# Kernel optimization log

Hardware: AMD Instinct MI355X
Metric: run time of the kernel (lower is better)

## Reference

```python
import jax, jax.numpy as jnp
import numpy as np

K = 10  # top-k from __init__ kwarg k


def _gru_cell(x, h, w_ih, w_hh, b_ih, b_hh):
    # torch nn.GRUCell gate order: r, z, n
    gi = x @ w_ih.T + b_ih
    gh = h @ w_hh.T + b_hh
    ir, iz, in_ = jnp.split(gi, 3, axis=-1)
    hr, hz, hn = jnp.split(gh, 3, axis=-1)
    r = jax.nn.sigmoid(ir + hr)
    z = jax.nn.sigmoid(iz + hz)
    n = jnp.tanh(in_ + r * hn)
    return (1.0 - z) * n + z * h


def setup_inputs() -> dict:
    key = jax.random.key(0)
    ks = jax.random.split(key, 10)
    B, V, H, L = 16, 50000, 512, 2
    E = H  # embedding_dim must equal rnn_size (embedding feeds GRU input)
    interesting = (jax.random.uniform(ks[0], (B, V)) < 0.01).astype(jnp.float32)
    masking = jnp.ones((B, V), jnp.float32)
    emb = jax.random.normal(ks[1], (V, E), jnp.float32) * 0.02
    s = 1.0 / np.sqrt(H)
    gw_ih = jax.random.normal(ks[2], (L, 3 * H, H), jnp.float32) * s
    gw_hh = jax.random.normal(ks[3], (L, 3 * H, H), jnp.float32) * s
    gb_ih = jax.random.normal(ks[4], (L, 3 * H), jnp.float32) * s
    gb_hh = jax.random.normal(ks[5], (L, 3 * H), jnp.float32) * s
    fc_w = jax.random.normal(ks[6], (V, H), jnp.float32) * s
    fc_b = jax.random.normal(ks[7], (V,), jnp.float32) * s
    value_w = jax.random.normal(ks[8], (1, H), jnp.float32) * s
    value_b = jax.random.normal(ks[9], (1,), jnp.float32) * s
    return {
        'user_interesting': interesting, 'user_masking': masking,
        'embedding': emb,
        'gru_w_ih': gw_ih, 'gru_w_hh': gw_hh, 'gru_b_ih': gb_ih, 'gru_b_hh': gb_hh,
        'fc_w': fc_w, 'fc_b': fc_b, 'value_w': value_w, 'value_b': value_b,
        'sequence_length': 32,
    }


def reference(user_interesting, user_masking, embedding, gru_w_ih, gru_w_hh,
              gru_b_ih, gru_b_hh, fc_w, fc_b, value_w, value_b, sequence_length):
    B, V = user_interesting.shape
    L, H = gru_w_ih.shape[0], value_w.shape[1]
    T = int(sequence_length)
    dt = user_interesting.dtype
    s_token, s_hit = 0, 1.0
    # NOTE (faithful to source): SimpleGRUCell.forward returns the OLD hidden
    # as new_state, so the recurrent state stays at its zero init every step.
    h0 = jnp.zeros((B, H), dt)
    # start inputs: embedding(start_token) * start_hit, broadcast over batch
    # (in torch the [1,E] input broadcasts against [B,H] hidden inside GRUCell;
    #  since hidden is zero this equals broadcasting the input to B).
    start_inputs = jnp.broadcast_to(embedding[s_token] * s_hit, (B, embedding.shape[1]))
    bidx = jnp.arange(B)[:, None]

    def step(carry, _):
        inputs, history = carry
        x = inputs
        for l in range(L):  # stacked GRU cells, hidden always zero (see note)
            x = _gru_cell(x, h0, gru_w_ih[l], gru_w_hh[l], gru_b_ih[l], gru_b_hh[l])
        policy = jax.nn.softmax(x @ fc_w.T + fc_b, axis=-1)        # [B,V]
        value = x @ value_w.T + value_b                             # [B,1]
        masked = policy * history
        _, topk_idx = jax.lax.top_k(masked, K)                      # [B,K]
        oh_topk = jnp.zeros_like(policy).at[bidx, topk_idx].set(1.0)
        cii = user_interesting * oh_topk
        hff = (jnp.sum(cii, axis=-1) > 0).astype(dt)[:, None]       # hit flag [B,1]
        score = hff * cii * policy + (1.0 - hff) * masked
        sel = jnp.argmax(score, axis=-1)                            # [B]
        oh_sel = jnp.zeros_like(policy).at[bidx, sel[:, None]].set(1.0)
        emb = embedding[sel]                                        # [B,E]
        next_inputs = hff * emb + (hff - 1.0) * emb                 # = (2*hff-1)*emb
        next_history = history - hff * oh_sel
        return (next_inputs, next_history), (policy, sel, value, hff)

    (_, final_history), (pol, sel, val, hit) = jax.lax.scan(
        step, (start_inputs, user_masking), None, length=T)
    # time-major -> batch-major
    logits = jnp.swapaxes(pol, 0, 1)        # [B,T,V]
    sample_ids = jnp.swapaxes(sel, 0, 1)    # [B,T]
    values = jnp.swapaxes(val, 0, 1)        # [B,T,1]
    hits = jnp.swapaxes(hit, 0, 1)          # [B,T,1]
    return logits, sample_ids, values, final_history, hits
```

## Files before the change

### kernel.cpp

```cpp
#include <hip/hip_runtime.h>


#define TT 32
#define BDIM 16
#define VD 50000
#define HD 512
#define NB3 782

#define WS_HIST 0
#define WS_X0   800000
#define WS_X1   808192
#define WS_X2T  816384
#define WS_SWS  824576
#define WS_TV   837088
#define WS_INVS 962208
#define WS_TI   962224
#define WS_FCWT 1088000

#define O_IDS 25600000
#define O_VAL 25600512
#define O_FH  25601024
#define O_HIT 26401024

__global__ __launch_bounds__(256) void k_init(const float4* __restrict__ mask4,
                                              const float4* __restrict__ emb4,
                                              float4* __restrict__ hist4,
                                              float4* __restrict__ x04)
{
    for (int idx = blockIdx.x * 256 + threadIdx.x; idx < 202048; idx += 256 * 256) {
        if (idx < 200000) hist4[idx] = mask4[idx];
        else { int c = idx - 200000; x04[c] = emb4[c & 127]; }
    }
}

__global__ __launch_bounds__(256) void k_transpose(const float* __restrict__ src,
                                                   float* __restrict__ dst)
{
    __shared__ float tile[64][65];
    const int bt = blockIdx.x, tv = bt >> 3, th = bt & 7;
    const int v0 = tv * 64, h0 = th * 64;
    const int tx = threadIdx.x & 63, ty4 = threadIdx.x >> 6;
    for (int p = 0; p < 16; p++) {
        int vr = p * 4 + ty4, v = v0 + vr;
        tile[vr][tx] = (v < VD) ? src[(size_t)v * HD + h0 + tx] : 0.f;
    }
    __syncthreads();
    for (int p = 0; p < 16; p++) {
        int hr = p * 4 + ty4, v = v0 + tx;
        if (v < VD) dst[(size_t)(h0 + hr) * VD + v] = tile[tx][hr];
    }
}

__global__ __launch_bounds__(256) void k_gru(const float* __restrict__ xin,
                                             float* __restrict__ xout,
                                             const float* __restrict__ W,
                                             const float* __restrict__ bi,
                                             const float* __restrict__ bh,
                                             int outT,
                                             float* __restrict__ dout,
                                             const float* __restrict__ invS,
                                             int tprev)
{
    if (blockIdx.x >= 128) {
        if (tprev < 0) return;
        for (int idx = (blockIdx.x - 128) * 256 + threadIdx.x; idx < 200000; idx += 256 * 256) {
            int b = idx / 12500, v4 = idx % 12500;
            float4* row = (float4*)(dout + ((size_t)b * TT + tprev) * VD);
            float4 e = row[v4]; float s = invS[b];
            e.x *= s; e.y *= s; e.z *= s; e.w *= s;
            row[v4] = e;
        }
        return;
    }
    const int tid = threadIdx.x;
    const int kq = tid & 3, b = (tid >> 2) & 15, jl = tid >> 6;
    const int j = blockIdx.x * 4 + jl;
    const float4* xr = (const float4*)(xin + (size_t)b * HD + kq * 128);
    const float4* wr = (const float4*)(W + (size_t)j * HD + kq * 128);
    const float4* wz = (const float4*)(W + (size_t)(j + 512) * HD + kq * 128);
    const float4* wn = (const float4*)(W + (size_t)(j + 1024) * HD + kq * 128);
    float4 aR = {0, 0, 0, 0}, aZ = {0, 0, 0, 0}, aN = {0, 0, 0, 0};
#pragma unroll 4
    for (int k = 0; k < 32; k++) {
        float4 x = xr[k];
        float4 r = wr[k];
        aR.x = fmaf(r.x, x.x, aR.x); aR.y = fmaf(r.y, x.y, aR.y);
        aR.z = fmaf(r.z, x.z, aR.z); aR.w = fmaf(r.w, x.w, aR.w);
        float4 z = wz[k];
        aZ.x = fmaf(z.x, x.x, aZ.x); aZ.y = fmaf(z.y, x.y, aZ.y);
        aZ.z = fmaf(z.z, x.z, aZ.z); aZ.w = fmaf(z.w, x.w, aZ.w);
        float4 n = wn[k];
        aN.x = fmaf(n.x, x.x, aN.x); aN.y = fmaf(n.y, x.y, aN.y);
        aN.z = fmaf(n.z, x.z, aN.z); aN.w = fmaf(n.w, x.w, aN.w);
    }
    float sR = (aR.x + aR.y) + (aR.z + aR.w);
    float sZ = (aZ.x + aZ.y) + (aZ.z + aZ.w);
    float sN = (aN.x + aN.y) + (aN.z + aN.w);
    sR += __shfl_xor(sR, 1, 64); sR += __shfl_xor(sR, 2, 64);
    sZ += __shfl_xor(sZ, 1, 64); sZ += __shfl_xor(sZ, 2, 64);
    sN += __shfl_xor(sN, 1, 64); sN += __shfl_xor(sN, 2, 64);
    if (kq == 0) {
        float gr = sR + bi[j] + bh[j];
        float gz = sZ + bi[512 + j] + bh[512 + j];
        float rr = 1.f / (1.f + expf(-gr));
        float zz = 1.f / (1.f + expf(-gz));
        float nn = tanhf(sN + bi[1024 + j] + rr * bh[1024 + j]);
        float o = (1.f - zz) * nn;
        if (outT) xout[(size_t)j * 16 + b] = o;
        else      xout[(size_t)b * HD + j] = o;
    }
}

template<int TRANS>
__global__ __launch_bounds__(256, 4) void k3_fc(const float* __restrict__ W,
                                                const float* __restrict__ fcb,
                                                const float* __restrict__ x2T,
                                                const float* __restrict__ hist,
                                                float* __restrict__ dout,
                                                float* __restrict__ s_ws,
                                                float* __restrict__ tv_ws,
                                                int* __restrict__ ti_ws,
                                                int t)
{
    __shared__ float red[4][64][17];
    __shared__ float elds[64][17];
    const int tid = threadIdx.x;
    const int wave = tid >> 6, lane = tid & 63;
    const int khu = __builtin_amdgcn_readfirstlane(wave);
    const int vb0 = blockIdx.x * 64;
    const int v = vb0 + lane;
    float acc[16];
#pragma unroll
    for (int i = 0; i < 16; i++) acc[i] = 0.f;
    const float* xp = x2T + khu * 128 * 16;
    if (v < VD) {
        if (TRANS) {
            const float* wp = W + (size_t)(khu * 128) * VD + v;
#pragma unroll 4
            for (int k = 0; k < 128; k++) {
                float w = wp[(size_t)k * VD];
                const float* xr = xp + k * 16;
#pragma unroll
                for (int bb = 0; bb < 16; bb++) acc[bb] = fmaf(w, xr[bb], acc[bb]);
            }
        } else {
            const float4* wp = (const float4*)(W + (size_t)v * HD + khu * 128);
#pragma unroll 2
            for (int k4 = 0; k4 < 32; k4++) {
                float4 w = wp[k4];
                const float* xr = xp + k4 * 64;
#pragma unroll
                for (int bb = 0; bb < 16; bb++) acc[bb] = fmaf(w.x, xr[bb], acc[bb]);
#pragma unroll
                for (int bb = 0; bb < 16; bb++) acc[bb] = fmaf(w.y, xr[16 + bb], acc[bb]);
#pragma unroll
                for (int bb = 0; bb < 16; bb++) acc[bb] = fmaf(w.z, xr[32 + bb], acc[bb]);
#pragma unroll
                for (int bb = 0; bb < 16; bb++) acc[bb] = fmaf(w.w, xr[48 + bb], acc[bb]);
            }
        }
    }
#pragma unroll
    for (int i = 0; i < 16; i++) red[khu][lane][i] = acc[i];
    __syncthreads();

    const int v_l = tid & 63;
    const int vglob = vb0 + v_l;
    const int bq = (tid >> 6) * 4;
    float fb = (vglob < VD) ? fcb[vglob] : 0.f;
#pragma unroll
    for (int q = 0; q < 4; q++) {
        int bb = bq + q;
        float lg = (red[0][v_l][bb] + red[1][v_l][bb]) + (red[2][v_l][bb] + red[3][v_l][bb]);
        float e = 0.f;
        if (vglob < VD) {
            e = expf(lg + fb);
            dout[((size_t)bb * TT + t) * VD + vglob] = e;
        }
        elds[v_l][bb] = e;
    }
    __syncthreads();

    for (int q = 0; q < 4; q++) {
        int bb = wave * 4 + q;
        float e0 = elds[lane][bb];
        float s = e0;
#pragma unroll
        for (int m = 1; m < 64; m <<= 1) s += __shfl_xor(s, m, 64);
        int i0 = vb0 + lane;
        float h0 = (i0 < VD) ? hist[(size_t)bb * VD + i0] : 0.f;
        float k0 = e0 * h0;
        for (int r = 0; r < 10; r++) {
            float cvv = k0; int cii = i0;
#pragma unroll
            for (int m = 1; m < 64; m <<= 1) {
                float ov = __shfl_xor(cvv, m, 64);
                int   oi = __shfl_xor(cii, m, 64);
                if (ov > cvv || (ov == cvv && oi < cii)) { cvv = ov; cii = oi; }
            }
            if (lane == 0) {
                size_t o = ((size_t)blockIdx.x * 16 + bb) * 10 + r;
                tv_ws[o] = cvv; ti_ws[o] = cii;
            }
            if (cii == i0) k0 = -1.f;
        }
        if (lane == 0) s_ws[blockIdx.x * 16 + bb] = s;
    }
}

__global__ __launch_bounds__(256) void k5_merge(const float* __restrict__ s_ws,
                                                const float* __restrict__ tv_ws,
                                                const int* __restrict__ ti_ws,
                                                const float* __restrict__ ui,
                                                const float* __restrict__ emb,
                                                const float* __restrict__ x2T,
                                                const float* __restrict__ vw,
                                                const float* __restrict__ vbias,
                                                float* __restrict__ hist,
                                                float* __restrict__ x0,
                                                float* __restrict__ dout,
                                                float* __restrict__ invS,
                                                int t)
{
    const int b = blockIdx.x, tid = threadIdx.x;
    __shared__ float cv[7824];
    __shared__ unsigned short ci16[7824];
    __shared__ float rv[256]; __shared__ int ri[256]; __shared__ int rs[256];
    __shared__ float t10v[10]; __shared__ int t10i[10];
    __shared__ float ifl[10], ev[10];
    __shared__ int s_sel; __shared__ float s_hff;

    for (int c = tid; c < 7820; c += 256) {
        int j = c / 10, r = c % 10;
        cv[c] = tv_ws[((size_t)j * 16 + b) * 10 + r];
        ci16[c] = (unsigned short)ti_ws[((size_t)j * 16 + b) * 10 + r];
    }
    if (tid < 4) { cv[7820 + tid] = -1e30f; ci16[7820 + tid] = 65535; }
    __syncthreads();

    for (int r = 0; r < 10; r++) {
        float bv = -1e30f; int bi = 0x7fffffff, bs = 0;
        for (int c = tid; c < 7820; c += 256) {
            float vv = cv[c]; int ii = (int)ci16[c];
            if (vv > bv || (vv == bv && ii < bi)) { bv = vv; bi = ii; bs = c; }
        }
        rv[tid] = bv; ri[tid] = bi; rs[tid] = bs;
        __syncthreads();
        for (int s = 128; s > 0; s >>= 1) {
            if (tid < s) {
                float ov = rv[tid + s]; int oi = ri[tid + s];
                if (ov > rv[tid] || (ov == rv[tid] && oi < ri[tid])) {
                    rv[tid] = ov; ri[tid] = oi; rs[tid] = rs[tid + s];
                }
            }
            __syncthreads();
        }
        if (tid == 0) { t10v[r] = rv[0]; t10i[r] = ri[0]; cv[rs[0]] = -1e30f; }
        __syncthreads();
    }

    float sp = 0.f;
    for (int c = tid; c < NB3; c += 256) sp += s_ws[c * 16 + b];
    rv[tid] = sp; __syncthreads();
    for (int s = 128; s > 0; s >>= 1) { if (tid < s) rv[tid] += rv[tid + s]; __syncthreads(); }
    float S = rv[0];
    __syncthreads();

    float vp = x2T[(size_t)tid * 16 + b] * vw[tid] + x2T[(size_t)(tid + 256) * 16 + b] * vw[tid + 256];
    rv[tid] = vp; __syncthreads();
    for (int s = 128; s > 0; s >>= 1) { if (tid < s) rv[tid] += rv[tid + s]; __syncthreads(); }

    if (tid < 10) {
        int ii = t10i[tid];
        ifl[tid] = ui[(size_t)b * VD + ii];
        ev[tid] = dout[((size_t)b * TT + t) * VD + ii];
    }
    __syncthreads();

    if (tid == 0) {
        int hff = 0; float bv = -1e30f; int bsel = -1;
        for (int r = 0; r < 10; r++) {
            if (ifl[r] != 0.f) {
                if (!hff || ev[r] > bv) { bv = ev[r]; bsel = t10i[r]; }
                hff = 1;
            }
        }
        int sel = hff ? bsel : t10i[0];
        s_sel = sel; s_hff = (float)hff;
        dout[O_IDS + b * TT + t] = (float)sel;
        dout[O_HIT + b * TT + t] = (float)hff;
        dout[O_VAL + b * TT + t] = rv[0] + vbias[0];
        invS[b] = 1.f / S;
        if (hff) hist[(size_t)b * VD + sel] -= 1.f;
    }
    __syncthreads();
    float f = 2.f * s_hff - 1.f;
    x0[(size_t)b * HD + tid]       = f * emb[(size_t)s_sel * HD + tid];
    x0[(size_t)b * HD + tid + 256] = f * emb[(size_t)s_sel * HD + tid + 256];
}

__global__ __launch_bounds__(256) void k_final(float* __restrict__ dout,
                                               const float4* __restrict__ hist4,
                                               const float* __restrict__ invS)
{
    for (int idx = blockIdx.x * 256 + threadIdx.x; idx < 400000; idx += 256 * 256) {
        if (idx < 200000) {
            int b = idx / 12500, v4 = idx % 12500;
            float4* row = (float4*)(dout + ((size_t)b * TT + 31) * VD);
            float4 e = row[v4]; float s = invS[b];
            e.x *= s; e.y *= s; e.z *= s; e.w *= s;
            row[v4] = e;
        } else {
            int c = idx - 200000;
            ((float4*)(dout + O_FH))[c] = hist4[c];
        }
    }
}

extern "C" void kernel_launch(void* const* d_in, const int* in_sizes, int n_in,
                              void* d_out, int out_size, void* d_ws, size_t ws_size,
                              hipStream_t stream)
{
    const float* ui   = (const float*)d_in[0];
    const float* mask = (const float*)d_in[1];
    const float* emb  = (const float*)d_in[2];
    const float* wih  = (const float*)d_in[3];
    const float* gbih = (const float*)d_in[5];
    const float* gbhh = (const float*)d_in[6];
    const float* fcw  = (const float*)d_in[7];
    const float* fcb  = (const float*)d_in[8];
    const float* vw   = (const float*)d_in[9];
    const float* vb   = (const float*)d_in[10];
    float* out = (float*)d_out;

    float* wsf  = (float*)d_ws;
    float* hist = wsf + WS_HIST;
    float* x0   = wsf + WS_X0;
    float* x1   = wsf + WS_X1;
    float* x2T  = wsf + WS_X2T;
    float* sws  = wsf + WS_SWS;
    float* tvws = wsf + WS_TV;
    float* invS = wsf + WS_INVS;
    int*   tiws = (int*)(wsf + WS_TI);
    float* fcwT = wsf + WS_FCWT;
    const bool use_t = ws_size >= (size_t)(WS_FCWT + (size_t)HD * VD) * 4;

    k_init<<<256, 256, 0, stream>>>((const float4*)mask, (const float4*)emb,
                                    (float4*)hist, (float4*)x0);
    if (use_t) k_transpose<<<6256, 256, 0, stream>>>(fcw, fcwT);

    for (int t = 0; t < TT; t++) {
        k_gru<<<384, 256, 0, stream>>>(x0, x1, wih, gbih, gbhh, 0, out, invS, t - 1);
        k_gru<<<128, 256, 0, stream>>>(x1, x2T, wih + 786432, gbih + 1536, gbhh + 1536,
                                       1, out, invS, -1);
        if (use_t) k3_fc<1><<<NB3, 256, 0, stream>>>(fcwT, fcb, x2T, hist, out, sws, tvws, tiws, t);
        else       k3_fc<0><<<NB3, 256, 0, stream>>>(fcw,  fcb, x2T, hist, out, sws, tvws, tiws, t);
        k5_merge<<<16, 256, 0, stream>>>(sws, tvws, tiws, ui, emb, x2T, vw, vb,
                                         hist, x0, out, invS, t);
    }
    k_final<<<256, 256, 0, stream>>>(out, (const float4*)hist, invS);
}
```

Baseline: 4.421 ms.

## Fuse layer-0 GRU into merge kernel and replace tree reductions with wave shuffles

Folds the first GRU layer of the next step into the top-k merge kernel. The 16 per-batch merge blocks become 64 blocks, each handling a quarter of the GRU output rows, so one kernel launch per step is removed and the selected embedding stays in shared memory. The previous-step logits rescale moves into the same kernel, and the step-0 layer-0 GRU moves into the init kernel. The shared-memory tree argmax reduction is replaced with wavefront shuffle reductions, which cuts barrier count. The cost is that each batch's top-10 selection is now computed four times redundantly.

```diff
diff --git a/kernel.cpp b/kernel.cpp
--- a/kernel.cpp
+++ b/kernel.cpp
@@ -2,13 +2,11 @@
 
 
 #define TT 32
-#define BDIM 16
 #define VD 50000
 #define HD 512
 #define NB3 782
 
 #define WS_HIST 0
-#define WS_X0   800000
 #define WS_X1   808192
 #define WS_X2T  816384
 #define WS_SWS  824576
@@ -23,13 +21,53 @@
 #define O_HIT 26401024
 
 __global__ __launch_bounds__(256) void k_init(const float4* __restrict__ mask4,
-                                              const float4* __restrict__ emb4,
                                               float4* __restrict__ hist4,
-                                              float4* __restrict__ x04)
-{
-    for (int idx = blockIdx.x * 256 + threadIdx.x; idx < 202048; idx += 256 * 256) {
-        if (idx < 200000) hist4[idx] = mask4[idx];
-        else { int c = idx - 200000; x04[c] = emb4[c & 127]; }
+                                              const float* __restrict__ emb,
+                                              const float* __restrict__ W,
+                                              const float* __restrict__ bi,
+                                              const float* __restrict__ bh,
+                                              float* __restrict__ x1)
+{
+    if (blockIdx.x < 256) {
+        for (int idx = blockIdx.x * 256 + threadIdx.x; idx < 200000; idx += 256 * 256)
+            hist4[idx] = mask4[idx];
+        return;
+    }
+    const int bid2 = blockIdx.x - 256;
+    const int tid = threadIdx.x;
+    const int kq = tid & 3, b = (tid >> 2) & 15, jl = tid >> 6;
+    const int j = bid2 * 4 + jl;
+    const float4* xr = (const float4*)(emb + kq * 128);
+    const float4* wr = (const float4*)(W + (size_t)j * HD + kq * 128);
+    const float4* wz = (const float4*)(W + (size_t)(j + 512) * HD + kq * 128);
+    const float4* wn = (const float4*)(W + (size_t)(j + 1024) * HD + kq * 128);
+    float4 aR = {0, 0, 0, 0}, aZ = {0, 0, 0, 0}, aN = {0, 0, 0, 0};
+#pragma unroll 4
+    for (int k = 0; k < 32; k++) {
+        float4 x = xr[k];
+        float4 r = wr[k];
+        aR.x = fmaf(r.x, x.x, aR.x); aR.y = fmaf(r.y, x.y, aR.y);
+        aR.z = fmaf(r.z, x.z, aR.z); aR.w = fmaf(r.w, x.w, aR.w);
+        float4 z = wz[k];
+        aZ.x = fmaf(z.x, x.x, aZ.x); aZ.y = fmaf(z.y, x.y, aZ.y);
+        aZ.z = fmaf(z.z, x.z, aZ.z); aZ.w = fmaf(z.w, x.w, aZ.w);
+        float4 n = wn[k];
+        aN.x = fmaf(n.x, x.x, aN.x); aN.y = fmaf(n.y, x.y, aN.y);
+        aN.z = fmaf(n.z, x.z, aN.z); aN.w = fmaf(n.w, x.w, aN.w);
+    }
+    float sR = (aR.x + aR.y) + (aR.z + aR.w);
+    float sZ = (aZ.x + aZ.y) + (aZ.z + aZ.w);
+    float sN = (aN.x + aN.y) + (aN.z + aN.w);
+    sR += __shfl_xor(sR, 1, 64); sR += __shfl_xor(sR, 2, 64);
+    sZ += __shfl_xor(sZ, 1, 64); sZ += __shfl_xor(sZ, 2, 64);
+    sN += __shfl_xor(sN, 1, 64); sN += __shfl_xor(sN, 2, 64);
+    if (kq == 0) {
+        float gr = sR + bi[j] + bh[j];
+        float gz = sZ + bi[512 + j] + bh[512 + j];
+        float rr = 1.f / (1.f + expf(-gr));
+        float zz = 1.f / (1.f + expf(-gz));
+        float nn = tanhf(sN + bi[1024 + j] + rr * bh[1024 + j]);
+        x1[(size_t)b * HD + j] = (1.f - zz) * nn;
     }
 }
 
@@ -51,27 +89,12 @@
     }
 }
 
-__global__ __launch_bounds__(256) void k_gru(const float* __restrict__ xin,
-                                             float* __restrict__ xout,
-                                             const float* __restrict__ W,
-                                             const float* __restrict__ bi,
-                                             const float* __restrict__ bh,
-                                             int outT,
-                                             float* __restrict__ dout,
-                                             const float* __restrict__ invS,
-                                             int tprev)
-{
-    if (blockIdx.x >= 128) {
-        if (tprev < 0) return;
-        for (int idx = (blockIdx.x - 128) * 256 + threadIdx.x; idx < 200000; idx += 256 * 256) {
-            int b = idx / 12500, v4 = idx % 12500;
-            float4* row = (float4*)(dout + ((size_t)b * TT + tprev) * VD);
-            float4 e = row[v4]; float s = invS[b];
-            e.x *= s; e.y *= s; e.z *= s; e.w *= s;
-            row[v4] = e;
-        }
-        return;
-    }
+__global__ __launch_bounds__(256) void k_gru1(const float* __restrict__ xin,
+                                              float* __restrict__ xout,
+                                              const float* __restrict__ W,
+                                              const float* __restrict__ bi,
+                                              const float* __restrict__ bh)
+{
     const int tid = threadIdx.x;
     const int kq = tid & 3, b = (tid >> 2) & 15, jl = tid >> 6;
     const int j = blockIdx.x * 4 + jl;
@@ -105,9 +128,7 @@
         float rr = 1.f / (1.f + expf(-gr));
         float zz = 1.f / (1.f + expf(-gz));
         float nn = tanhf(sN + bi[1024 + j] + rr * bh[1024 + j]);
-        float o = (1.f - zz) * nn;
-        if (outT) xout[(size_t)j * 16 + b] = o;
-        else      xout[(size_t)b * HD + j] = o;
+        xout[(size_t)j * 16 + b] = (1.f - zz) * nn;
     }
 }
 
@@ -208,72 +229,96 @@
     }
 }
 
-__global__ __launch_bounds__(256) void k5_merge(const float* __restrict__ s_ws,
-                                                const float* __restrict__ tv_ws,
-                                                const int* __restrict__ ti_ws,
-                                                const float* __restrict__ ui,
-                                                const float* __restrict__ emb,
-                                                const float* __restrict__ x2T,
-                                                const float* __restrict__ vw,
-                                                const float* __restrict__ vbias,
-                                                float* __restrict__ hist,
-                                                float* __restrict__ x0,
-                                                float* __restrict__ dout,
-                                                float* __restrict__ invS,
-                                                int t)
-{
-    const int b = blockIdx.x, tid = threadIdx.x;
+__global__ __launch_bounds__(256) void k_mergeall(const float* __restrict__ s_ws,
+                                                  const float* __restrict__ tv_ws,
+                                                  const int* __restrict__ ti_ws,
+                                                  const float* __restrict__ ui,
+                                                  const float* __restrict__ emb,
+                                                  const float* __restrict__ x2T,
+                                                  const float* __restrict__ vw,
+                                                  const float* __restrict__ vbias,
+                                                  float* __restrict__ hist,
+                                                  float* __restrict__ x1out,
+                                                  const float* __restrict__ W0,
+                                                  const float* __restrict__ bi0,
+                                                  const float* __restrict__ bh0,
+                                                  float* __restrict__ dout,
+                                                  float* __restrict__ invS,
+                                                  int t)
+{
+    const int tid = threadIdx.x;
+    if (blockIdx.x >= 64) {
+        if (t == 0) return;
+        for (int idx = (blockIdx.x - 64) * 256 + tid; idx < 200000; idx += 256 * 256) {
+            int b = idx / 12500, v4 = idx % 12500;
+            float4* row = (float4*)(dout + ((size_t)b * TT + (t - 1)) * VD);
+            float4 e = row[v4]; float s = invS[b];
+            e.x *= s; e.y *= s; e.z *= s; e.w *= s;
+            row[v4] = e;
+        }
+        return;
+    }
+    const int b = blockIdx.x >> 2, jq = blockIdx.x & 3;
     __shared__ float cv[7824];
     __shared__ unsigned short ci16[7824];
-    __shared__ float rv[256]; __shared__ int ri[256]; __shared__ int rs[256];
+    __shared__ float rv[256];
+    __shared__ float wbv[4]; __shared__ int wbi[4]; __shared__ int wbs[4];
     __shared__ float t10v[10]; __shared__ int t10i[10];
     __shared__ float ifl[10], ev[10];
     __shared__ int s_sel; __shared__ float s_hff;
+    __shared__ __align__(16) float x0b[512];
 
     for (int c = tid; c < 7820; c += 256) {
         int j = c / 10, r = c % 10;
         cv[c] = tv_ws[((size_t)j * 16 + b) * 10 + r];
         ci16[c] = (unsigned short)ti_ws[((size_t)j * 16 + b) * 10 + r];
     }
-    if (tid < 4) { cv[7820 + tid] = -1e30f; ci16[7820 + tid] = 65535; }
-    __syncthreads();
-
+    __syncthreads();
+
+    const int lane = tid & 63, wv = tid >> 6;
     for (int r = 0; r < 10; r++) {
         float bv = -1e30f; int bi = 0x7fffffff, bs = 0;
         for (int c = tid; c < 7820; c += 256) {
             float vv = cv[c]; int ii = (int)ci16[c];
             if (vv > bv || (vv == bv && ii < bi)) { bv = vv; bi = ii; bs = c; }
         }
-        rv[tid] = bv; ri[tid] = bi; rs[tid] = bs;
+#pragma unroll
+        for (int m = 1; m < 64; m <<= 1) {
+            float ov = __shfl_xor(bv, m, 64);
+            int   oi = __shfl_xor(bi, m, 64);
+            int   os = __shfl_xor(bs, m, 64);
+            if (ov > bv || (ov == bv && oi < bi)) { bv = ov; bi = oi; bs = os; }
+        }
+        if (lane == 0) { wbv[wv] = bv; wbi[wv] = bi; wbs[wv] = bs; }
         __syncthreads();
-        for (int s = 128; s > 0; s >>= 1) {
-            if (tid < s) {
-                float ov = rv[tid + s]; int oi = ri[tid + s];
-                if (ov > rv[tid] || (ov == rv[tid] && oi < ri[tid])) {
-                    rv[tid] = ov; ri[tid] = oi; rs[tid] = rs[tid + s];
-                }
-            }
-            __syncthreads();
-        }
-        if (tid == 0) { t10v[r] = rv[0]; t10i[r] = ri[0]; cv[rs[0]] = -1e30f; }
+        if (tid == 0) {
+            float fv = wbv[0]; int fi = wbi[0], fs = wbs[0];
+#pragma unroll
+            for (int w = 1; w < 4; w++)
+                if (wbv[w] > fv || (wbv[w] == fv && wbi[w] < fi)) { fv = wbv[w]; fi = wbi[w]; fs = wbs[w]; }
+            t10v[r] = fv; t10i[r] = fi; cv[fs] = -1e30f;
+        }
         __syncthreads();
     }
 
-    float sp = 0.f;
-    for (int c = tid; c < NB3; c += 256) sp += s_ws[c * 16 + b];
-    rv[tid] = sp; __syncthreads();
-    for (int s = 128; s > 0; s >>= 1) { if (tid < s) rv[tid] += rv[tid + s]; __syncthreads(); }
-    float S = rv[0];
-    __syncthreads();
-
-    float vp = x2T[(size_t)tid * 16 + b] * vw[tid] + x2T[(size_t)(tid + 256) * 16 + b] * vw[tid + 256];
-    rv[tid] = vp; __syncthreads();
-    for (int s = 128; s > 0; s >>= 1) { if (tid < s) rv[tid] += rv[tid + s]; __syncthreads(); }
+    float S_reg = 0.f;
+    if (jq == 0) {
+        float sp = 0.f;
+        for (int c = tid; c < NB3; c += 256) sp += s_ws[c * 16 + b];
+        rv[tid] = sp; __syncthreads();
+        for (int s = 128; s > 0; s >>= 1) { if (tid < s) rv[tid] += rv[tid + s]; __syncthreads(); }
+        S_reg = rv[0];
+        __syncthreads();
+        float vp = x2T[(size_t)tid * 16 + b] * vw[tid]
+                 + x2T[(size_t)(tid + 256) * 16 + b] * vw[tid + 256];
+        rv[tid] = vp; __syncthreads();
+        for (int s = 128; s > 0; s >>= 1) { if (tid < s) rv[tid] += rv[tid + s]; __syncthreads(); }
+    }
 
     if (tid < 10) {
         int ii = t10i[tid];
         ifl[tid] = ui[(size_t)b * VD + ii];
-        ev[tid] = dout[((size_t)b * TT + t) * VD + ii];
+        ev[tid]  = dout[((size_t)b * TT + t) * VD + ii];
     }
     __syncthreads();
 
@@ -287,16 +332,60 @@
         }
         int sel = hff ? bsel : t10i[0];
         s_sel = sel; s_hff = (float)hff;
-        dout[O_IDS + b * TT + t] = (float)sel;
-        dout[O_HIT + b * TT + t] = (float)hff;
-        dout[O_VAL + b * TT + t] = rv[0] + vbias[0];
-        invS[b] = 1.f / S;
-        if (hff) hist[(size_t)b * VD + sel] -= 1.f;
-    }
-    __syncthreads();
-    float f = 2.f * s_hff - 1.f;
-    x0[(size_t)b * HD + tid]       = f * emb[(size_t)s_sel * HD + tid];
-    x0[(size_t)b * HD + tid + 256] = f * emb[(size_t)s_sel * HD + tid + 256];
+        if (jq == 0) {
+            dout[O_IDS + b * TT + t] = (float)sel;
+            dout[O_HIT + b * TT + t] = (float)hff;
+            dout[O_VAL + b * TT + t] = rv[0] + vbias[0];
+            invS[b] = 1.f / S_reg;
+            if (hff) hist[(size_t)b * VD + sel] -= 1.f;
+        }
+    }
+    __syncthreads();
+
+    if (t < 31) {
+        float f = 2.f * s_hff - 1.f;
+        int sel = s_sel;
+        x0b[tid]       = f * emb[(size_t)sel * HD + tid];
+        x0b[tid + 256] = f * emb[(size_t)sel * HD + tid + 256];
+        __syncthreads();
+        const int kq = tid & 3, jl = tid >> 2;
+        const float4* xr = (const float4*)(x0b + kq * 128);
+#pragma unroll
+        for (int jp = 0; jp < 2; jp++) {
+            const int j = jq * 128 + jp * 64 + jl;
+            const float4* wr = (const float4*)(W0 + (size_t)j * HD + kq * 128);
+            const float4* wz = (const float4*)(W0 + (size_t)(j + 512) * HD + kq * 128);
+            const float4* wn = (const float4*)(W0 + (size_t)(j + 1024) * HD + kq * 128);
+            float4 aR = {0, 0, 0, 0}, aZ = {0, 0, 0, 0}, aN = {0, 0, 0, 0};
+#pragma unroll 4
+            for (int k = 0; k < 32; k++) {
+                float4 x = xr[k];
+                float4 rr4 = wr[k];
+                aR.x = fmaf(rr4.x, x.x, aR.x); aR.y = fmaf(rr4.y, x.y, aR.y);
+                aR.z = fmaf(rr4.z, x.z, aR.z); aR.w = fmaf(rr4.w, x.w, aR.w);
+                float4 zz4 = wz[k];
+                aZ.x = fmaf(zz4.x, x.x, aZ.x); aZ.y = fmaf(zz4.y, x.y, aZ.y);
+                aZ.z = fmaf(zz4.z, x.z, aZ.z); aZ.w = fmaf(zz4.w, x.w, aZ.w);
+                float4 nn4 = wn[k];
+                aN.x = fmaf(nn4.x, x.x, aN.x); aN.y = fmaf(nn4.y, x.y, aN.y);
+                aN.z = fmaf(nn4.z, x.z, aN.z); aN.w = fmaf(nn4.w, x.w, aN.w);
+            }
+            float sR = (aR.x + aR.y) + (aR.z + aR.w);
+            float sZ = (aZ.x + aZ.y) + (aZ.z + aZ.w);
+            float sN = (aN.x + aN.y) + (aN.z + aN.w);
+            sR += __shfl_xor(sR, 1, 64); sR += __shfl_xor(sR, 2, 64);
+            sZ += __shfl_xor(sZ, 1, 64); sZ += __shfl_xor(sZ, 2, 64);
+            sN += __shfl_xor(sN, 1, 64); sN += __shfl_xor(sN, 2, 64);
+            if (kq == 0) {
+                float gr = sR + bi0[j] + bh0[j];
+                float gz = sZ + bi0[512 + j] + bh0[512 + j];
+                float rr = 1.f / (1.f + expf(-gr));
+                float zz = 1.f / (1.f + expf(-gz));
+                float nn = tanhf(sN + bi0[1024 + j] + rr * bh0[1024 + j]);
+                x1out[(size_t)b * HD + j] = (1.f - zz) * nn;
+            }
+        }
+    }
 }
 
 __global__ __launch_bounds__(256) void k_final(float* __restrict__ dout,
@@ -335,7 +424,6 @@
 
     float* wsf  = (float*)d_ws;
     float* hist = wsf + WS_HIST;
-    float* x0   = wsf + WS_X0;
     float* x1   = wsf + WS_X1;
     float* x2T  = wsf + WS_X2T;
     float* sws  = wsf + WS_SWS;
@@ -345,18 +433,18 @@
     float* fcwT = wsf + WS_FCWT;
     const bool use_t = ws_size >= (size_t)(WS_FCWT + (size_t)HD * VD) * 4;
 
-    k_init<<<256, 256, 0, stream>>>((const float4*)mask, (const float4*)emb,
-                                    (float4*)hist, (float4*)x0);
+    k_init<<<384, 256, 0, stream>>>((const float4*)mask, (float4*)hist,
+                                    emb, wih, gbih, gbhh, x1);
     if (use_t) k_transpose<<<6256, 256, 0, stream>>>(fcw, fcwT);
+    k_gru1<<<128, 256, 0, stream>>>(x1, x2T, wih + 786432, gbih + 1536, gbhh + 1536);
 
     for (int t = 0; t < TT; t++) {
-        k_gru<<<384, 256, 0, stream>>>(x0, x1, wih, gbih, gbhh, 0, out, invS, t - 1);
-        k_gru<<<128, 256, 0, stream>>>(x1, x2T, wih + 786432, gbih + 1536, gbhh + 1536,
-                                       1, out, invS, -1);
         if (use_t) k3_fc<1><<<NB3, 256, 0, stream>>>(fcwT, fcb, x2T, hist, out, sws, tvws, tiws, t);
         else       k3_fc<0><<<NB3, 256, 0, stream>>>(fcw,  fcb, x2T, hist, out, sws, tvws, tiws, t);
-        k5_merge<<<16, 256, 0, stream>>>(sws, tvws, tiws, ui, emb, x2T, vw, vb,
-                                         hist, x0, out, invS, t);
+        k_mergeall<<<320, 256, 0, stream>>>(sws, tvws, tiws, ui, emb, x2T, vw, vb,
+                                            hist, x1, wih, gbih, gbhh, out, invS, t);
+        if (t < 31)
+            k_gru1<<<128, 256, 0, stream>>>(x1, x2T, wih + 786432, gbih + 1536, gbhh + 1536);
     }
     k_final<<<256, 256, 0, stream>>>(out, (const float4*)hist, invS);
 }
```

Result: no change. 4.440 ms (+0.4%).
